# Kernel optimization log

Measured on AMD Instinct MI355X. Metric: run time of the kernel, lower is better.

The kernel has to match this reference:

```python
import jax, jax.numpy as jnp
import numpy as np


@jax.custom_vjp
def binarize_ste(x):
    return jnp.sign(x)


def _binarize_fwd(x):
    return jnp.sign(x), None


def _binarize_bwd(_, g):
    # straight-through estimator: pass gradient through, clamped to [-1, 1]
    return (jnp.clip(g, -1.0, 1.0),)


binarize_ste.defvjp(_binarize_fwd, _binarize_bwd)


def setup_inputs() -> dict:
    key = jax.random.key(0)
    kx, kw = jax.random.split(key)
    x = jax.random.normal(kx, (32, 128, 64, 64), dtype=jnp.float32)  # NCHW
    weight = jax.random.normal(kw, (256, 128, 3, 3), dtype=jnp.float32)  # OIHW
    return {"x": x, "weight": weight}


def reference(x, weight):
    w_bin = binarize_ste(weight)  # +/-1 (0 where weight==0, matching torch.sign)
    out = jax.lax.conv_general_dilated(
        x, w_bin,
        window_strides=(1, 1),
        padding=((1, 1), (1, 1)),
        dimension_numbers=("NCHW", "OIHW", "NCHW"),
    )
    return out
```

## Files before the change

kernel.cpp:

```cpp
#include <hip/hip_runtime.h>
#include <hip/hip_bf16.h>


typedef short bf16x8 __attribute__((ext_vector_type(8)));
typedef float f32x4 __attribute__((ext_vector_type(4)));

#define XT_ELEMS (32 * 66 * 66 * 128)
#define XT_BYTES (XT_ELEMS * 2)

__device__ __forceinline__ void glds16(const void* g, const void* l) {
    __builtin_amdgcn_global_load_lds(
        (const __attribute__((address_space(1))) void*)g,
        (__attribute__((address_space(3))) void*)l, 16, 0, 0);
}

__global__ void prep_w_kernel(const float* __restrict__ w,
                              __hip_bfloat16* __restrict__ wm) {
    int tid = blockIdx.x * 256 + threadIdx.x;
    int o = tid / 1152;
    int r = tid - o * 1152;
    int j = r >> 7;
    int c = r & 127;
    float v = w[o * 1152 + c * 9 + j];
    float s = (v > 0.f) ? 1.f : ((v < 0.f) ? -1.f : 0.f);
    wm[tid] = __float2bfloat16(s);
}

__global__ void transpose_x_kernel(const float* __restrict__ x,
                                   __hip_bfloat16* __restrict__ xt) {
    __shared__ short tl[64 * 130];
    const int t = threadIdx.x;
    const int n = blockIdx.x >> 6;
    const int h = blockIdx.x & 63;
    const float* xp = x + (size_t)n * 524288 + h * 64;
    for (int i = t; i < 8192; i += 256) {
        int w = i & 63, c = i >> 6;
        tl[w * 130 + c] = (short)__bfloat16_as_ushort(__float2bfloat16(xp[c * 4096 + w]));
    }
    uint* xtn = (uint*)(xt + (size_t)n * 66 * 66 * 128);
    {
        int row = h + 1;
        if (t < 64)       xtn[(row * 66 + 0) * 64 + t] = 0u;
        else if (t < 128) xtn[(row * 66 + 65) * 64 + (t - 64)] = 0u;
    }
    if (h == 0)  for (int i = t; i < 66 * 64; i += 256) xtn[i] = 0u;
    if (h == 63) for (int i = t; i < 66 * 64; i += 256) xtn[65 * 66 * 64 + i] = 0u;
    __syncthreads();
    uint* xo = (uint*)(xt + ((size_t)(n * 66 + h + 1) * 66 + 1) * 128);
    for (int i = t; i < 4096; i += 256) {
        int c2 = i & 63;
        int w = i >> 6;
        xo[w * 64 + c2] = *(const uint*)(tl + w * 130 + c2 * 2);
    }
}

__global__ __launch_bounds__(256, 2) void gemm_kernel(
    const __hip_bfloat16* __restrict__ xt,
    const __hip_bfloat16* __restrict__ wm,
    float* __restrict__ out) {
    __shared__ short As[128 * 64];
    __shared__ short Bw[2112 * 8];

    const int t = threadIdx.x;
    const int lane = t & 63;
    const int wv = t >> 6;
    const int px_blk = blockIdx.x;
    const int o_blk = blockIdx.y;
    const int n = px_blk >> 4;
    const int h0 = (px_blk & 15) * 4;

    const int wo = (wv & 1) * 64;
    const int wp = (wv >> 1) * 128;
    const int wpr = wp >> 6;
    const int l15 = lane & 15;
    const int quad = lane >> 4;
    const int srow = lane >> 3;
    const int sseg = lane & 7;

    const short* wmS = (const short*)wm + (o_blk * 128) * 1152;
    const short* xtS = (const short*)xt;

    f32x4 acc[4][8] = {};

    for (int cc = 0; cc < 128; cc += 64) {
        for (int kh = 0; kh < 3; ++kh) {
            const short* xw = xtS + ((size_t)(n * 66 + h0 + kh) * 66) * 128;
#pragma unroll
            for (int i = 0; i < 9; ++i) {
                int bidx = i * 4 + wv;
                if (bidx < 33) {
                    int l = bidx * 64 + lane;
                    int cell = l >> 3;
                    int q = l & 7;
                    int s = q ^ (cell & 7);
                    glds16(xw + cell * 128 + cc + s * 8, Bw + bidx * 512);
                }
            }
            for (int kw = 0; kw < 3; ++kw) {
                const int j = kh * 3 + kw;
#pragma unroll
                for (int i = 0; i < 4; ++i) {
                    int r0 = wv * 32 + i * 8;
                    int r = r0 + srow;
                    int segl = sseg ^ (r & 7);
                    glds16(wmS + r * 1152 + j * 128 + cc + segl * 8,
                           As + r0 * 64);
                }
                __syncthreads();
#pragma unroll
                for (int kf = 0; kf < 2; ++kf) {
                    bf16x8 a[4], b[8];
#pragma unroll
                    for (int i = 0; i < 4; ++i) {
                        int o = wo + i * 16 + l15;
                        int seg = (kf * 4 + quad) ^ (o & 7);
                        a[i] = *(const bf16x8*)(As + o * 64 + seg * 8);
                    }
#pragma unroll
                    for (int i = 0; i < 8; ++i) {
                        int cell = (wpr + (i >> 2)) * 66 + (i & 3) * 16 + l15 + kw;
                        int seg = (kf * 4 + quad) ^ (cell & 7);
                        b[i] = *(const bf16x8*)(Bw + cell * 64 + seg * 8);
                    }
#pragma unroll
                    for (int i = 0; i < 4; ++i)
#pragma unroll
                        for (int jj = 0; jj < 8; ++jj)
                            acc[i][jj] = __builtin_amdgcn_mfma_f32_16x16x32_bf16(
                                a[i], b[jj], acc[i][jj], 0, 0, 0);
                }
                __syncthreads();
            }
        }
    }

    const int Pbase = px_blk * 256 + wp;
#pragma unroll
    for (int i = 0; i < 4; ++i) {
#pragma unroll
        for (int jj = 0; jj < 8; ++jj) {
            const int P = Pbase + jj * 16 + l15;
            const int hw = P & 4095;
            float* op = out + (size_t)n * 1048576 + hw;
#pragma unroll
            for (int r = 0; r < 4; ++r) {
                const int o = o_blk * 128 + wo + i * 16 + quad * 4 + r;
                op[(size_t)o * 4096] = acc[i][jj][r];
            }
        }
    }
}

extern "C" void kernel_launch(void* const* d_in, const int* in_sizes, int n_in,
                              void* d_out, int out_size, void* d_ws, size_t ws_size,
                              hipStream_t stream) {
    const float* x = (const float*)d_in[0];
    const float* w = (const float*)d_in[1];
    float* out = (float*)d_out;
    __hip_bfloat16* xt = (__hip_bfloat16*)d_ws;
    __hip_bfloat16* wm = (__hip_bfloat16*)((char*)d_ws + XT_BYTES);

    prep_w_kernel<<<1152, 256, 0, stream>>>(w, wm);
    transpose_x_kernel<<<2048, 256, 0, stream>>>(x, xt);
    gemm_kernel<<<dim3(512, 2), 256, 0, stream>>>(xt, wm, out);
}
```

Measured before the change: 248.4 us.

## Preload weights in MFMA fragment layout and stage full 6-row input halo once

Weights are pre-permuted into MFMA A-fragment order so each lane loads its bf16x8 operand straight from global memory, which removes the LDS staging of A and the per-tap barriers. The input tile now covers all 6 padded rows (400 cells) and is loaded into LDS once per channel half instead of once per kh, so only one or two barriers remain per block. The transpose kernel also switches to wider float2 and uint2 accesses. The cost is that A operands come from global or cache on every tap and kw step, which adds load latency, and LDS use goes up to about 51KB, which may affect occupancy at 2 blocks per CU.

```diff
diff --git a/kernel.cpp b/kernel.cpp
--- a/kernel.cpp
+++ b/kernel.cpp
@@ -7,6 +7,7 @@
 
 #define XT_ELEMS (32 * 66 * 66 * 128)
 #define XT_BYTES (XT_ELEMS * 2)
+#define XT_PAD_BYTES (66 * 128 * 2)
 
 __device__ __forceinline__ void glds16(const void* g, const void* l) {
     __builtin_amdgcn_global_load_lds(
@@ -15,15 +16,20 @@
 }
 
 __global__ void prep_w_kernel(const float* __restrict__ w,
-                              __hip_bfloat16* __restrict__ wm) {
+                              __hip_bfloat16* __restrict__ af) {
     int tid = blockIdx.x * 256 + threadIdx.x;
-    int o = tid / 1152;
-    int r = tid - o * 1152;
-    int j = r >> 7;
-    int c = r & 127;
+    int e = tid & 7;
+    int l15 = (tid >> 3) & 15;
+    int quad = (tid >> 7) & 3;
+    int o16 = (tid >> 9) & 15;
+    int kf = (tid >> 13) & 1;
+    int ccI = (tid >> 14) & 1;
+    int j = tid >> 15;
+    int o = o16 * 16 + l15;
+    int c = ccI * 64 + kf * 32 + quad * 8 + e;
     float v = w[o * 1152 + c * 9 + j];
     float s = (v > 0.f) ? 1.f : ((v < 0.f) ? -1.f : 0.f);
-    wm[tid] = __float2bfloat16(s);
+    af[tid] = __float2bfloat16(s);
 }
 
 __global__ void transpose_x_kernel(const float* __restrict__ x,
@@ -33,9 +39,11 @@
     const int n = blockIdx.x >> 6;
     const int h = blockIdx.x & 63;
     const float* xp = x + (size_t)n * 524288 + h * 64;
-    for (int i = t; i < 8192; i += 256) {
-        int w = i & 63, c = i >> 6;
-        tl[w * 130 + c] = (short)__bfloat16_as_ushort(__float2bfloat16(xp[c * 4096 + w]));
+    for (int i = t; i < 4096; i += 256) {
+        int w2 = i & 31, c = i >> 5;
+        float2 v = *(const float2*)(xp + c * 4096 + w2 * 2);
+        tl[(w2 * 2 + 0) * 130 + c] = (short)__bfloat16_as_ushort(__float2bfloat16(v.x));
+        tl[(w2 * 2 + 1) * 130 + c] = (short)__bfloat16_as_ushort(__float2bfloat16(v.y));
     }
     uint* xtn = (uint*)(xt + (size_t)n * 66 * 66 * 128);
     {
@@ -46,20 +54,22 @@
     if (h == 0)  for (int i = t; i < 66 * 64; i += 256) xtn[i] = 0u;
     if (h == 63) for (int i = t; i < 66 * 64; i += 256) xtn[65 * 66 * 64 + i] = 0u;
     __syncthreads();
-    uint* xo = (uint*)(xt + ((size_t)(n * 66 + h + 1) * 66 + 1) * 128);
-    for (int i = t; i < 4096; i += 256) {
-        int c2 = i & 63;
-        int w = i >> 6;
-        xo[w * 64 + c2] = *(const uint*)(tl + w * 130 + c2 * 2);
+    uint2* xo = (uint2*)(xt + ((size_t)(n * 66 + h + 1) * 66 + 1) * 128);
+    for (int i = t; i < 2048; i += 256) {
+        int c4 = i & 31;
+        int w = i >> 5;
+        uint2 v;
+        v.x = *(const uint*)(tl + w * 130 + c4 * 4);
+        v.y = *(const uint*)(tl + w * 130 + c4 * 4 + 2);
+        xo[w * 32 + c4] = v;
     }
 }
 
 __global__ __launch_bounds__(256, 2) void gemm_kernel(
     const __hip_bfloat16* __restrict__ xt,
-    const __hip_bfloat16* __restrict__ wm,
+    const __hip_bfloat16* __restrict__ af,
     float* __restrict__ out) {
-    __shared__ short As[128 * 64];
-    __shared__ short Bw[2112 * 8];
+    __shared__ short Bw[400 * 64];
 
     const int t = threadIdx.x;
     const int lane = t & 63;
@@ -74,51 +84,41 @@
     const int wpr = wp >> 6;
     const int l15 = lane & 15;
     const int quad = lane >> 4;
-    const int srow = lane >> 3;
-    const int sseg = lane & 7;
 
-    const short* wmS = (const short*)wm + (o_blk * 128) * 1152;
-    const short* xtS = (const short*)xt;
+    const short* xw = (const short*)xt + (size_t)(n * 66 + h0) * 66 * 128;
+    const short* afp = (const short*)af;
+    const int o16base = o_blk * 8 + (wv & 1) * 4;
 
     f32x4 acc[4][8] = {};
 
-    for (int cc = 0; cc < 128; cc += 64) {
+#pragma unroll 1
+    for (int ccI = 0; ccI < 2; ++ccI) {
+        if (ccI) __syncthreads();
+#pragma unroll
+        for (int m = wv; m < 50; m += 4) {
+            int s = m * 64 + lane;
+            int cel = s >> 3;
+            int q = s & 7;
+            int sg = q ^ (cel & 7);
+            glds16(xw + cel * 128 + ccI * 64 + sg * 8, Bw + m * 512);
+        }
+        __syncthreads();
+#pragma unroll 1
         for (int kh = 0; kh < 3; ++kh) {
-            const short* xw = xtS + ((size_t)(n * 66 + h0 + kh) * 66) * 128;
 #pragma unroll
-            for (int i = 0; i < 9; ++i) {
-                int bidx = i * 4 + wv;
-                if (bidx < 33) {
-                    int l = bidx * 64 + lane;
-                    int cell = l >> 3;
-                    int q = l & 7;
-                    int s = q ^ (cell & 7);
-                    glds16(xw + cell * 128 + cc + s * 8, Bw + bidx * 512);
-                }
-            }
             for (int kw = 0; kw < 3; ++kw) {
                 const int j = kh * 3 + kw;
-#pragma unroll
-                for (int i = 0; i < 4; ++i) {
-                    int r0 = wv * 32 + i * 8;
-                    int r = r0 + srow;
-                    int segl = sseg ^ (r & 7);
-                    glds16(wmS + r * 1152 + j * 128 + cc + segl * 8,
-                           As + r0 * 64);
-                }
-                __syncthreads();
 #pragma unroll
                 for (int kf = 0; kf < 2; ++kf) {
                     bf16x8 a[4], b[8];
 #pragma unroll
                     for (int i = 0; i < 4; ++i) {
-                        int o = wo + i * 16 + l15;
-                        int seg = (kf * 4 + quad) ^ (o & 7);
-                        a[i] = *(const bf16x8*)(As + o * 64 + seg * 8);
+                        int fragIdx = ((j * 2 + ccI) * 2 + kf) * 16 + o16base + i;
+                        a[i] = *(const bf16x8*)(afp + fragIdx * 512 + lane * 8);
                     }
 #pragma unroll
                     for (int i = 0; i < 8; ++i) {
-                        int cell = (wpr + (i >> 2)) * 66 + (i & 3) * 16 + l15 + kw;
+                        int cell = (kh + wpr + (i >> 2)) * 66 + (i & 3) * 16 + l15 + kw;
                         int seg = (kf * 4 + quad) ^ (cell & 7);
                         b[i] = *(const bf16x8*)(Bw + cell * 64 + seg * 8);
                     }
@@ -129,7 +129,6 @@
                             acc[i][jj] = __builtin_amdgcn_mfma_f32_16x16x32_bf16(
                                 a[i], b[jj], acc[i][jj], 0, 0, 0);
                 }
-                __syncthreads();
             }
         }
     }
@@ -158,9 +157,9 @@
     const float* w = (const float*)d_in[1];
     float* out = (float*)d_out;
     __hip_bfloat16* xt = (__hip_bfloat16*)d_ws;
-    __hip_bfloat16* wm = (__hip_bfloat16*)((char*)d_ws + XT_BYTES);
+    __hip_bfloat16* af = (__hip_bfloat16*)((char*)d_ws + XT_BYTES + XT_PAD_BYTES);
 
-    prep_w_kernel<<<1152, 256, 0, stream>>>(w, wm);
+    prep_w_kernel<<<1152, 256, 0, stream>>>(w, af);
     transpose_x_kernel<<<2048, 256, 0, stream>>>(x, xt);
-    gemm_kernel<<<dim3(512, 2), 256, 0, stream>>>(xt, wm, out);
+    gemm_kernel<<<dim3(512, 2), 256, 0, stream>>>(xt, af, out);
 }
```

Measured after the change: 254.9 us. +2.6%, slower.
